# Performance work log

Measured on AMD Instinct MI355X. Metric: run time of the kernel, lower is better.

Reference implementation:

```python
import jax, jax.numpy as jnp
import numpy as np

SCALE = 0.02  # weight init scale to keep activations sane


def setup_inputs() -> dict:
    key = jax.random.key(0)
    ks = jax.random.split(key, 6)
    B, T, C = 4, 2048, 2048
    NB, BS, R = 16, 128, 128  # n_diag_blocks, diag_blocksize, rank
    x = jax.random.normal(ks[0], (B, T, C), dtype=jnp.float32)
    diag = jax.random.normal(ks[1], (4, NB, BS, BS), dtype=jnp.float32) * SCALE
    left_w = jax.random.normal(ks[2], (4, R, C), dtype=jnp.float32) * SCALE   # Linear(in=C, out=R).weight
    right_w = jax.random.normal(ks[3], (4, C, R), dtype=jnp.float32) * SCALE  # Linear(in=R, out=C).weight
    right_b = jax.random.normal(ks[4], (4, C), dtype=jnp.float32) * SCALE
    bias_p = jax.random.normal(ks[5], (4, C), dtype=jnp.float32) * SCALE
    return {"x": x, "diag": diag, "left_w": left_w, "right_w": right_w,
            "right_b": right_b, "bias_p": bias_p, "n_head": 16}


def _lori_fc(x, diag_i, left_i, right_w_i, right_b_i, bias_i):
    # x: [B,T,C]; block-diagonal path done as batched per-block matmul
    B, T, C = x.shape
    nb, bs, _ = diag_i.shape
    x1 = jnp.einsum('btnd,nde->btne', x.reshape(B, T, nb, bs), diag_i).reshape(B, T, C)
    # low-rank path: right(left(x)) with right bias
    x2 = jnp.einsum('btr,cr->btc', jnp.einsum('btc,rc->btr', x, left_i), right_w_i) + right_b_i
    return x1 + x2 + bias_i  # module's own bias (bias=True)


def reference(x, diag, left_w, right_w, right_b, bias_p, n_head):
    B, T, C = x.shape
    hd = C // n_head
    q = _lori_fc(x, diag[0], left_w[0], right_w[0], right_b[0], bias_p[0])
    k = _lori_fc(x, diag[1], left_w[1], right_w[1], right_b[1], bias_p[1])
    v = _lori_fc(x, diag[2], left_w[2], right_w[2], right_b[2], bias_p[2])
    # [B, H, T, hd]
    q = q.reshape(B, T, n_head, hd).transpose(0, 2, 1, 3)
    k = k.reshape(B, T, n_head, hd).transpose(0, 2, 1, 3)
    v = v.reshape(B, T, n_head, hd).transpose(0, 2, 1, 3)
    att = jnp.einsum('bhqd,bhkd->bhqk', q, k) * (1.0 / jnp.sqrt(jnp.float32(hd)))
    causal = jnp.tril(jnp.ones((T, T), dtype=bool))
    att = jnp.where(causal, att, jnp.finfo(att.dtype).min)
    att = jax.nn.softmax(att, axis=-1)
    y = jnp.einsum('bhqk,bhkd->bhqd', att, v)
    y = y.transpose(0, 2, 1, 3).reshape(B, T, C)
    y = _lori_fc(y, diag[3], left_w[3], right_w[3], right_b[3], bias_p[3])
    return y
```

## Files before the change

kernel.cpp:

```cpp
#include <hip/hip_runtime.h>

typedef short bf16x8 __attribute__((ext_vector_type(8)));
typedef short bf16x4 __attribute__((ext_vector_type(4)));
typedef float f32x4  __attribute__((ext_vector_type(4)));

#define AS1 __attribute__((address_space(1)))
#define AS3 __attribute__((address_space(3)))

__device__ __forceinline__ void gload16(const void* g, void* l) {
  __builtin_amdgcn_global_load_lds((const AS1 void*)g, (AS3 void*)l, 16, 0, 0);
}

__device__ __forceinline__ short f2bf(float f) {
  union { float fv; unsigned u; } v; v.fv = f;
  unsigned r = v.u + 0x7fffu + ((v.u >> 16) & 1u);
  return (short)(r >> 16);
}

__device__ __forceinline__ short f2bf_t(float f) {
  return (short)(__float_as_uint(f) >> 16);
}

__global__ void cast_prep_kernel(const float* __restrict__ x, const float* __restrict__ left_w,
                                 const float* __restrict__ diag, const float* __restrict__ right_w,
                                 short* __restrict__ xb, short* __restrict__ LT, short* __restrict__ WT) {
  long idx = (long)blockIdx.x * 256 + threadIdx.x;
  const long N4 = 4194304L;
  const long LTN = 4L * 128 * 2048;
  const long WTN = 4L * 16 * 128 * 256;
  if (idx < N4) {
    float4 v = ((const float4*)x)[idx];
    short4 s;
    s.x = f2bf(v.x); s.y = f2bf(v.y); s.z = f2bf(v.z); s.w = f2bf(v.w);
    ((short4*)xb)[idx] = s;
  } else if (idx < N4 + LTN) {
    long j = idx - N4;
    LT[j] = f2bf(left_w[j]);
  } else if (idx < N4 + LTN + WTN) {
    long j = idx - N4 - LTN;
    int d = (int)(j & 255);
    long rest = j >> 8;
    int e = (int)(rest & 127);
    long gi = rest >> 7;
    int i = (int)(gi >> 4), n = (int)(gi & 15);
    float v;
    if (d < 128) v = diag[(gi * 128 + d) * 128 + e];
    else         v = right_w[((long)i * 2048 + n * 128 + e) * 128 + (d - 128)];
    WT[j] = f2bf(v);
  }
}

__global__ __launch_bounds__(256) void gemm_bt(const short* __restrict__ A, const short* __restrict__ BT,
                                               short* __restrict__ C, int M, int N, int K) {
  __shared__ __align__(16) short As[2][128 * 64];
  __shared__ __align__(16) short Bs[2][128 * 64];
  int tid = threadIdx.x, w = tid >> 6, lane = tid & 63;
  int m0 = blockIdx.x * 128, n0 = blockIdx.y * 128;
  int wm = (w >> 1) * 64, wn = (w & 1) * 64;
  int quad = lane >> 4, l16 = lane & 15;
  int srow = lane >> 3;
  int schunk = ((lane & 7) ^ srow) * 8;

#define GSTAGE(K0, BUF) {                                                             \
    for (int p = 0; p < 4; ++p) {                                                     \
      int r = p * 32 + w * 8 + srow;                                                  \
      gload16(&A[(long)(m0 + r) * K + (K0) + schunk], &As[BUF][(p * 32 + w * 8) * 64]); \
      gload16(&BT[(long)(n0 + r) * K + (K0) + schunk], &Bs[BUF][(p * 32 + w * 8) * 64]); \
    }                                                                                 \
  }

  f32x4 acc[4][4] = {};
  GSTAGE(0, 0)
  __syncthreads();
  int nk = K >> 6;
  for (int it = 0; it < nk; ++it) {
    int cur = it & 1;
    if (it + 1 < nk) GSTAGE((it + 1) * 64, cur ^ 1)
#pragma unroll
    for (int kk = 0; kk < 2; ++kk) {
      int c = (((kk * 4 + quad) ^ (l16 & 7)) * 8);
      bf16x8 a[4], b[4];
#pragma unroll
      for (int t = 0; t < 4; ++t) a[t] = *(const bf16x8*)&As[cur][(wm + t * 16 + l16) * 64 + c];
#pragma unroll
      for (int t = 0; t < 4; ++t) b[t] = *(const bf16x8*)&Bs[cur][(wn + t * 16 + l16) * 64 + c];
#pragma unroll
      for (int mt = 0; mt < 4; ++mt)
#pragma unroll
        for (int nt = 0; nt < 4; ++nt)
          acc[mt][nt] = __builtin_amdgcn_mfma_f32_16x16x32_bf16(a[mt], b[nt], acc[mt][nt], 0, 0, 0);
    }
    __syncthreads();
  }
#undef GSTAGE
#pragma unroll
  for (int mt = 0; mt < 4; ++mt)
#pragma unroll
    for (int nt = 0; nt < 4; ++nt)
#pragma unroll
      for (int r = 0; r < 4; ++r) {
        int m = m0 + wm + mt * 16 + quad * 4 + r;
        int n = n0 + wn + nt * 16 + l16;
        C[(long)m * N + n] = f2bf(acc[mt][nt][r]);
      }
}

__global__ __launch_bounds__(256) void lori_gemm(const short* __restrict__ tok, const short* __restrict__ rnk,
                                                 int rstride, const short* __restrict__ WT,
                                                 const float* __restrict__ rb, const float* __restrict__ bp,
                                                 int i_base, short* __restrict__ qb, short* __restrict__ kb,
                                                 short* __restrict__ vT, float* __restrict__ out) {
  __shared__ __align__(16) short As[2][128 * 64];
  __shared__ __align__(16) short Bs[2][128 * 64];
  int tid = threadIdx.x, w = tid >> 6, lane = tid & 63;
  int i = i_base + (blockIdx.y >> 4);
  int n = blockIdx.y & 15;
  int t0 = blockIdx.x * 128;
  int co = (i < 3) ? i * 128 : 0;
  const short* WTn = WT + (long)(i * 16 + n) * 128 * 256;
  int wm = (w >> 1) * 64, wn = (w & 1) * 64;
  int quad = lane >> 4, l16 = lane & 15;
  int srow = lane >> 3;
  int schunk = ((lane & 7) ^ srow) * 8;

#define LSTAGE(KT, BUF) {                                                             \
    for (int p = 0; p < 4; ++p) {                                                     \
      int r = p * 32 + w * 8 + srow;                                                  \
      const short* ga;                                                                \
      if ((KT) < 2) ga = &tok[(long)(t0 + r) * 2048 + n * 128 + (KT) * 64 + schunk];  \
      else          ga = &rnk[(long)(t0 + r) * rstride + co + ((KT) - 2) * 64 + schunk]; \
      gload16(ga, &As[BUF][(p * 32 + w * 8) * 64]);                                   \
      gload16(&WTn[r * 256 + (KT) * 64 + schunk], &Bs[BUF][(p * 32 + w * 8) * 64]);   \
    }                                                                                 \
  }

  f32x4 acc[4][4] = {};
  LSTAGE(0, 0)
  __syncthreads();
#pragma unroll
  for (int kt = 0; kt < 4; ++kt) {
    int cur = kt & 1;
    if (kt < 3) LSTAGE(kt + 1, cur ^ 1)
#pragma unroll
    for (int kk = 0; kk < 2; ++kk) {
      int c = (((kk * 4 + quad) ^ (l16 & 7)) * 8);
      bf16x8 a[4], b[4];
#pragma unroll
      for (int t = 0; t < 4; ++t) a[t] = *(const bf16x8*)&As[cur][(wm + t * 16 + l16) * 64 + c];
#pragma unroll
      for (int t = 0; t < 4; ++t) b[t] = *(const bf16x8*)&Bs[cur][(wn + t * 16 + l16) * 64 + c];
#pragma unroll
      for (int mt = 0; mt < 4; ++mt)
#pragma unroll
        for (int nt = 0; nt < 4; ++nt)
          acc[mt][nt] = __builtin_amdgcn_mfma_f32_16x16x32_bf16(a[mt], b[nt], acc[mt][nt], 0, 0, 0);
    }
    __syncthreads();
  }
#undef LSTAGE
  int b = t0 >> 11;
  int tl0 = t0 & 2047;
  const float QSC = 0.08838834764831845f * 1.4426950408889634f;
#pragma unroll
  for (int mt = 0; mt < 4; ++mt) {
#pragma unroll
    for (int nt = 0; nt < 4; ++nt) {
      int e = wn + nt * 16 + l16;
      int c = n * 128 + e;
      float bias = rb[i * 2048 + c] + bp[i * 2048 + c];
      int tl = tl0 + wm + mt * 16 + quad * 4;
      if (i == 0) {
#pragma unroll
        for (int r = 0; r < 4; ++r)
          qb[((long)(b * 16 + n) * 2048 + tl + r) * 128 + e] = f2bf((acc[mt][nt][r] + bias) * QSC);
      } else if (i == 1) {
#pragma unroll
        for (int r = 0; r < 4; ++r)
          kb[((long)(b * 16 + n) * 2048 + tl + r) * 128 + e] = f2bf(acc[mt][nt][r] + bias);
      } else if (i == 2) {
        short4 s4;
        s4.x = f2bf(acc[mt][nt][0] + bias);
        s4.y = f2bf(acc[mt][nt][1] + bias);
        s4.z = f2bf(acc[mt][nt][2] + bias);
        s4.w = f2bf(acc[mt][nt][3] + bias);
        *(short4*)&vT[((long)(b * 16 + n) * 128 + e) * 2048 + tl] = s4;
      } else {
#pragma unroll
        for (int r = 0; r < 4; ++r)
          out[(long)(t0 + wm + mt * 16 + quad * 4 + r) * 2048 + c] = acc[mt][nt][r] + bias;
      }
    }
  }
}

__global__ __launch_bounds__(512, 3) void attn_kernel(const short* __restrict__ qb, const short* __restrict__ kb,
                                                      const short* __restrict__ vT, short* __restrict__ y) {
  __shared__ __align__(16) short ks[2][64 * 128];
  __shared__ __align__(16) short vs[2][128 * 64];
  int tid = threadIdx.x, w = tid >> 6, lane = tid & 63;
  int id = blockIdx.x;
  int xcd = id & 7;
  int sl = (id >> 3) & 31;
  int round = id >> 8;
  int bh = xcd + 8 * (sl & 7);
  int qt = round ? (sl >> 3) : 7 - (sl >> 3);
  int b = bh >> 4, h = bh & 15;
  int quad = lane >> 4, l16 = lane & 15;

  bf16x8 aq[2][4];
#pragma unroll
  for (int mt = 0; mt < 2; ++mt)
#pragma unroll
    for (int kk = 0; kk < 4; ++kk)
      aq[mt][kk] = *(const bf16x8*)&qb[((long)bh * 2048 + qt * 256 + w * 32 + mt * 16 + l16) * 128 + kk * 32 + quad * 8];

  f32x4 O[2][8] = {};
  f32x4 Lacc[2] = {};
  float mst[2] = {-3.0e38f, -3.0e38f};
  const bf16x4 ones4 = {(short)0x3F80, (short)0x3F80, (short)0x3F80, (short)0x3F80};

  int kq = lane >> 4;
  int kchunk = l16 ^ ((w * 4 + kq) & 15);
  int vrow8 = lane >> 3;
  int vchunk = (lane & 7) ^ (vrow8 & 7);

  const short* kbase = kb + (long)bh * 2048 * 128;
  const short* vbase = vT + (long)bh * 128 * 2048;

#define STAGE(JT, BUF) {                                                              \
    for (int p = 0; p < 2; ++p) {                                                     \
      int r = p * 32 + w * 4 + kq;                                                    \
      gload16(&kbase[((long)((JT) * 64 + r)) * 128 + kchunk * 8], &ks[BUF][(p * 32 + w * 4) * 128]); \
      int r2 = p * 64 + w * 8 + vrow8;                                                \
      gload16(&vbase[(long)r2 * 2048 + (JT) * 64 + vchunk * 8], &vs[BUF][(p * 64 + w * 8) * 64]);    \
    }                                                                                 \
  }

  int jmax_w = 4 * qt + (w >> 1);
  int jtend = 4 * qt + 3;
  STAGE(0, 0)
  __syncthreads();
  for (int jt = 0; jt <= jtend; ++jt) {
    int cur = jt & 1;
    if (jt < jtend) STAGE(jt + 1, cur ^ 1)

    if (jt <= jmax_w) {
      f32x4 s[2][4] = {};
#pragma unroll
      for (int nt = 0; nt < 4; ++nt)
#pragma unroll
        for (int kk = 0; kk < 4; ++kk) {
          bf16x8 bk = *(const bf16x8*)&ks[cur][(nt * 16 + l16) * 128 + (((kk * 4 + quad) ^ l16) * 8)];
          s[0][nt] = __builtin_amdgcn_mfma_f32_16x16x32_bf16(bk, aq[0][kk], s[0][nt], 0, 0, 0);
          s[1][nt] = __builtin_amdgcn_mfma_f32_16x16x32_bf16(bk, aq[1][kk], s[1][nt], 0, 0, 0);
        }
      if (jt == jmax_w) {
#pragma unroll
        for (int mt = 0; mt < 2; ++mt)
#pragma unroll
          for (int nt = 0; nt < 4; ++nt) {
            int q = qt * 256 + w * 32 + mt * 16 + l16;
#pragma unroll
            for (int r = 0; r < 4; ++r) {
              int key = jt * 64 + nt * 16 + quad * 4 + r;
              if (key > q) s[mt][nt][r] = -3.0e38f;
            }
          }
      }
      bf16x4 pb[2][4];
#pragma unroll
      for (int mt = 0; mt < 2; ++mt) {
        f32x4 vm;
#pragma unroll
        for (int r = 0; r < 4; ++r)
          vm[r] = fmaxf(fmaxf(s[mt][0][r], s[mt][1][r]), fmaxf(s[mt][2][r], s[mt][3][r]));
        float mx = fmaxf(fmaxf(vm[0], vm[1]), fmaxf(vm[2], vm[3]));
        mx = fmaxf(mx, __shfl_xor(mx, 16));
        mx = fmaxf(mx, __shfl_xor(mx, 32));
        float nm = fmaxf(mst[mt], mx);
        float al = __builtin_amdgcn_exp2f(mst[mt] - nm);
        mst[mt] = nm;
        Lacc[mt] *= al;
#pragma unroll
        for (int dt = 0; dt < 8; ++dt) O[mt][dt] *= al;
#pragma unroll
        for (int nt = 0; nt < 4; ++nt) {
          bf16x4 p;
#pragma unroll
          for (int r = 0; r < 4; ++r) p[r] = f2bf_t(__builtin_amdgcn_exp2f(s[mt][nt][r] - nm));
          pb[mt][nt] = p;
        }
      }
#pragma unroll
      for (int nt = 0; nt < 4; ++nt) {
        int coff = ((nt * 2 + (quad >> 1)) ^ (l16 & 7)) * 8 + (quad & 1) * 4;
        bf16x4 av[8];
#pragma unroll
        for (int dt = 0; dt < 8; ++dt) av[dt] = *(const bf16x4*)&vs[cur][(dt * 16 + l16) * 64 + coff];
#pragma unroll
        for (int mt = 0; mt < 2; ++mt) {
#pragma unroll
          for (int dt = 0; dt < 8; ++dt)
            O[mt][dt] = __builtin_amdgcn_mfma_f32_16x16x16bf16_1k(av[dt], pb[mt][nt], O[mt][dt], 0, 0, 0);
          Lacc[mt] = __builtin_amdgcn_mfma_f32_16x16x16bf16_1k(ones4, pb[mt][nt], Lacc[mt], 0, 0, 0);
        }
      }
    }
    __syncthreads();
  }
#undef STAGE
#pragma unroll
  for (int mt = 0; mt < 2; ++mt) {
    float inv = __builtin_amdgcn_rcpf(Lacc[mt][0]);
    int q = qt * 256 + w * 32 + mt * 16 + l16;
#pragma unroll
    for (int dt = 0; dt < 8; ++dt) {
      short4 s4;
      s4.x = f2bf(O[mt][dt][0] * inv);
      s4.y = f2bf(O[mt][dt][1] * inv);
      s4.z = f2bf(O[mt][dt][2] * inv);
      s4.w = f2bf(O[mt][dt][3] * inv);
      *(short4*)&y[((long)(b * 2048 + q)) * 2048 + h * 128 + dt * 16 + quad * 4] = s4;
    }
  }
}

extern "C" void kernel_launch(void* const* d_in, const int* in_sizes, int n_in,
                              void* d_out, int out_size, void* d_ws, size_t ws_size,
                              hipStream_t stream) {
  const float* x       = (const float*)d_in[0];
  const float* diag    = (const float*)d_in[1];
  const float* left_w  = (const float*)d_in[2];
  const float* right_w = (const float*)d_in[3];
  const float* right_b = (const float*)d_in[4];
  const float* bias_p  = (const float*)d_in[5];
  float* out = (float*)d_out;

  char* ws = (char*)d_ws;
  short* xb = (short*)(ws + 0);
  short* LT = (short*)(ws + 33554432);
  short* WT = (short*)(ws + 35651584);
  short* xl = (short*)(ws + 39845888);
  short* yl = (short*)(ws + 46137344);
  short* qb = (short*)(ws + 48234496);
  short* kb = (short*)(ws + 81788928);
  short* vT = (short*)(ws + 115343360);
  short* y  = xb;

  cast_prep_kernel<<<28672, 256, 0, stream>>>(x, left_w, diag, right_w, xb, LT, WT);
  gemm_bt<<<dim3(64, 3), 256, 0, stream>>>(xb, LT, xl, 8192, 384, 2048);
  lori_gemm<<<dim3(64, 48), 256, 0, stream>>>(xb, xl, 384, WT, right_b, bias_p, 0, qb, kb, vT, nullptr);
  attn_kernel<<<dim3(512), 512, 0, stream>>>(qb, kb, vT, y);
  gemm_bt<<<dim3(64, 1), 256, 0, stream>>>(y, LT + 3L * 128 * 2048, yl, 8192, 128, 2048);
  lori_gemm<<<dim3(64, 16), 256, 0, stream>>>(y, yl, 128, WT, right_b, bias_p, 3, nullptr, nullptr, nullptr, out);
}
```

Measured before the change: 435.9 us.

## Shrink attention blocks to 128 queries and drop K/V double buffering

```diff
diff --git a/kernel.cpp b/kernel.cpp
--- a/kernel.cpp
+++ b/kernel.cpp
@@ -193,17 +193,14 @@
   }
 }
 
-__global__ __launch_bounds__(512, 3) void attn_kernel(const short* __restrict__ qb, const short* __restrict__ kb,
+__global__ __launch_bounds__(256, 4) void attn_kernel(const short* __restrict__ qb, const short* __restrict__ kb,
                                                       const short* __restrict__ vT, short* __restrict__ y) {
-  __shared__ __align__(16) short ks[2][64 * 128];
-  __shared__ __align__(16) short vs[2][128 * 64];
+  __shared__ __align__(16) short ks[64 * 128];
+  __shared__ __align__(16) short vs[128 * 64];
   int tid = threadIdx.x, w = tid >> 6, lane = tid & 63;
   int id = blockIdx.x;
-  int xcd = id & 7;
-  int sl = (id >> 3) & 31;
-  int round = id >> 8;
-  int bh = xcd + 8 * (sl & 7);
-  int qt = round ? (sl >> 3) : 7 - (sl >> 3);
+  int bh = id & 63;
+  int qt = (int)((0x5410672398DCABEFULL >> ((id >> 6) * 4)) & 15);
   int b = bh >> 4, h = bh & 15;
   int quad = lane >> 4, l16 = lane & 15;
 
@@ -212,7 +209,7 @@
   for (int mt = 0; mt < 2; ++mt)
 #pragma unroll
     for (int kk = 0; kk < 4; ++kk)
-      aq[mt][kk] = *(const bf16x8*)&qb[((long)bh * 2048 + qt * 256 + w * 32 + mt * 16 + l16) * 128 + kk * 32 + quad * 8];
+      aq[mt][kk] = *(const bf16x8*)&qb[((long)bh * 2048 + qt * 128 + w * 32 + mt * 16 + l16) * 128 + kk * 32 + quad * 8];
 
   f32x4 O[2][8] = {};
   f32x4 Lacc[2] = {};
@@ -220,29 +217,28 @@
   const bf16x4 ones4 = {(short)0x3F80, (short)0x3F80, (short)0x3F80, (short)0x3F80};
 
   int kq = lane >> 4;
-  int kchunk = l16 ^ ((w * 4 + kq) & 15);
   int vrow8 = lane >> 3;
   int vchunk = (lane & 7) ^ (vrow8 & 7);
 
   const short* kbase = kb + (long)bh * 2048 * 128;
   const short* vbase = vT + (long)bh * 128 * 2048;
 
-#define STAGE(JT, BUF) {                                                              \
-    for (int p = 0; p < 2; ++p) {                                                     \
-      int r = p * 32 + w * 4 + kq;                                                    \
-      gload16(&kbase[((long)((JT) * 64 + r)) * 128 + kchunk * 8], &ks[BUF][(p * 32 + w * 4) * 128]); \
-      int r2 = p * 64 + w * 8 + vrow8;                                                \
-      gload16(&vbase[(long)r2 * 2048 + (JT) * 64 + vchunk * 8], &vs[BUF][(p * 64 + w * 8) * 64]);    \
+#define STAGE(JT) {                                                                   \
+    for (int p = 0; p < 4; ++p) {                                                     \
+      int r = w * 16 + p * 4 + kq;                                                    \
+      int kch = l16 ^ ((p * 4 + kq) & 15);                                            \
+      gload16(&kbase[((long)((JT) * 64 + r)) * 128 + kch * 8], &ks[(w * 16 + p * 4) * 128]); \
+      int r2 = w * 32 + p * 8 + vrow8;                                                \
+      gload16(&vbase[(long)r2 * 2048 + (JT) * 64 + vchunk * 8], &vs[(w * 32 + p * 8) * 64]); \
     }                                                                                 \
   }
 
-  int jmax_w = 4 * qt + (w >> 1);
-  int jtend = 4 * qt + 3;
-  STAGE(0, 0)
-  __syncthreads();
+  int jmax_w = 2 * qt + (w >> 1);
+  int jtend = 2 * qt + 1;
   for (int jt = 0; jt <= jtend; ++jt) {
-    int cur = jt & 1;
-    if (jt < jtend) STAGE(jt + 1, cur ^ 1)
+    if (jt) __syncthreads();
+    STAGE(jt)
+    __syncthreads();
 
     if (jt <= jmax_w) {
       f32x4 s[2][4] = {};
@@ -250,7 +246,7 @@
       for (int nt = 0; nt < 4; ++nt)
 #pragma unroll
         for (int kk = 0; kk < 4; ++kk) {
-          bf16x8 bk = *(const bf16x8*)&ks[cur][(nt * 16 + l16) * 128 + (((kk * 4 + quad) ^ l16) * 8)];
+          bf16x8 bk = *(const bf16x8*)&ks[(nt * 16 + l16) * 128 + (((kk * 4 + quad) ^ l16) * 8)];
           s[0][nt] = __builtin_amdgcn_mfma_f32_16x16x32_bf16(bk, aq[0][kk], s[0][nt], 0, 0, 0);
           s[1][nt] = __builtin_amdgcn_mfma_f32_16x16x32_bf16(bk, aq[1][kk], s[1][nt], 0, 0, 0);
         }
@@ -259,7 +255,7 @@
         for (int mt = 0; mt < 2; ++mt)
 #pragma unroll
           for (int nt = 0; nt < 4; ++nt) {
-            int q = qt * 256 + w * 32 + mt * 16 + l16;
+            int q = qt * 128 + w * 32 + mt * 16 + l16;
 #pragma unroll
             for (int r = 0; r < 4; ++r) {
               int key = jt * 64 + nt * 16 + quad * 4 + r;
@@ -296,7 +292,7 @@
         int coff = ((nt * 2 + (quad >> 1)) ^ (l16 & 7)) * 8 + (quad & 1) * 4;
         bf16x4 av[8];
 #pragma unroll
-        for (int dt = 0; dt < 8; ++dt) av[dt] = *(const bf16x4*)&vs[cur][(dt * 16 + l16) * 64 + coff];
+        for (int dt = 0; dt < 8; ++dt) av[dt] = *(const bf16x4*)&vs[(dt * 16 + l16) * 64 + coff];
 #pragma unroll
         for (int mt = 0; mt < 2; ++mt) {
 #pragma unroll
@@ -306,13 +302,12 @@
         }
       }
     }
-    __syncthreads();
   }
 #undef STAGE
 #pragma unroll
   for (int mt = 0; mt < 2; ++mt) {
     float inv = __builtin_amdgcn_rcpf(Lacc[mt][0]);
-    int q = qt * 256 + w * 32 + mt * 16 + l16;
+    int q = qt * 128 + w * 32 + mt * 16 + l16;
 #pragma unroll
     for (int dt = 0; dt < 8; ++dt) {
       short4 s4;
@@ -350,7 +345,7 @@
   cast_prep_kernel<<<28672, 256, 0, stream>>>(x, left_w, diag, right_w, xb, LT, WT);
   gemm_bt<<<dim3(64, 3), 256, 0, stream>>>(xb, LT, xl, 8192, 384, 2048);
   lori_gemm<<<dim3(64, 48), 256, 0, stream>>>(xb, xl, 384, WT, right_b, bias_p, 0, qb, kb, vT, nullptr);
-  attn_kernel<<<dim3(512), 512, 0, stream>>>(qb, kb, vT, y);
+  attn_kernel<<<dim3(1024), 256, 0, stream>>>(qb, kb, vT, y);
   gemm_bt<<<dim3(64, 1), 256, 0, stream>>>(y, LT + 3L * 128 * 2048, yl, 8192, 128, 2048);
   lori_gemm<<<dim3(64, 16), 256, 0, stream>>>(y, yl, 128, WT, right_b, bias_p, 3, nullptr, nullptr, nullptr, out);
 }
```

Measured after the change: 765.4 us. 1.76x slower.
